# Kernel optimization log

Measured on AMD Instinct MI355X. Metric: run time of the kernel, lower is better.

The kernel has to match this reference:

```python
import jax, jax.numpy as jnp
import numpy as np

H = 4  # num_heads


def _ln(x, g, b, eps=1e-5):
    m = x.mean(-1, keepdims=True)
    v = ((x - m) ** 2).mean(-1, keepdims=True)
    return (x - m) / jnp.sqrt(v + eps) * g + b


def setup_inputs() -> dict:
    key = jax.random.key(0)
    ks = jax.random.split(key, 16)
    B, N, M, dQ, dK, dV = 4, 2048, 2048, 128, 128, 128
    s = 0.02
    return {
        "Q": jax.random.normal(ks[0], (B, N, dQ), jnp.float32),
        "K": jax.random.normal(ks[1], (B, M, dK), jnp.float32),
        "adj_mask": jax.random.randint(ks[2], (B, N, M), 0, 2, jnp.int32),
        "Wq": jax.random.normal(ks[3], (dQ, dV), jnp.float32) * s,
        "bq": jnp.zeros((dV,), jnp.float32),
        "Wk": jax.random.normal(ks[4], (dK, dV), jnp.float32) * s,
        "bk": jnp.zeros((dV,), jnp.float32),
        "Wv": jax.random.normal(ks[5], (dK, dV), jnp.float32) * s,
        "bv": jnp.zeros((dV,), jnp.float32),
        "Wr1": jax.random.normal(ks[6], (dV, dV), jnp.float32) * s,
        "br1": jnp.zeros((dV,), jnp.float32),
        "Wr2": jax.random.normal(ks[7], (dV, dV), jnp.float32) * s,
        "br2": jnp.zeros((dV,), jnp.float32),
        "g0": jnp.ones((dV,), jnp.float32),
        "be0": jnp.zeros((dV,), jnp.float32),
        "g1": jnp.ones((dV,), jnp.float32),
        "be1": jnp.zeros((dV,), jnp.float32),
    }


def reference(Q, K, adj_mask, Wq, bq, Wk, bk, Wv, bv, Wr1, br1, Wr2, br2, g0, be0, g1, be1):
    B, N, _ = Q.shape
    M = K.shape[1]
    dV = Wq.shape[1]
    dh = dV // H
    Qp = Q @ Wq + bq   # [B,N,dV]
    Kp = K @ Wk + bk   # [B,M,dV]
    Vp = K @ Wv + bv   # [B,M,dV]
    # torch: split dim_V into H chunks, cat along dim 0 -> head-major [H*B, L, dh]
    def to_heads(x, L):
        return x.reshape(B, L, H, dh).transpose(2, 0, 1, 3).reshape(H * B, L, dh)
    Qh, Kh, Vh = to_heads(Qp, N), to_heads(Kp, M), to_heads(Vp, M)
    attn = jnp.einsum('bnd,bmd->bnm', Qh, Kh) / jnp.sqrt(jnp.float32(dh))  # [H*B,N,M]
    # torch repeat_interleave(mask, H, dim=0) gives batch-major order -- faithful
    mask = jnp.repeat(adj_mask, H, axis=0)
    attn = jnp.where(mask == 0, -jnp.inf, attn)
    A = jax.nn.softmax(attn, axis=2)
    O = Qh + jnp.einsum('bnm,bmd->bnd', A, Vh)  # [H*B,N,dh]
    # recombine heads back to [B,N,dV] (intended split(dim=0)/cat(dim=2))
    O = O.reshape(H, B, N, dh).transpose(1, 2, 0, 3).reshape(B, N, dV)
    O = _ln(O, g0, be0)
    O = O + (jax.nn.relu(O @ Wr1 + br1) @ Wr2 + br2)
    return _ln(O, g1, be1)
```

## Files before the change

kernel.cpp:

```cpp
#include <hip/hip_runtime.h>
#include <hip/hip_bf16.h>


typedef short bf16x8 __attribute__((ext_vector_type(8)));
typedef float f32x4 __attribute__((ext_vector_type(4)));

#define BN 4
#define SEQ 2048
#define DIM 128
#define NH 4
#define DH 32
#define ROWS (BN * SEQ)
#define MS 4
#define MWORDS (SEQ / 32)

static __device__ __forceinline__ unsigned short f2bf(float f) {
    __hip_bfloat16 h = __float2bfloat16(f);
    return *reinterpret_cast<unsigned short*>(&h);
}
static __device__ __forceinline__ float bf2f(unsigned short u) {
    union { unsigned int i; float f; } cv;
    cv.i = ((unsigned int)u) << 16;
    return cv.f;
}
static __device__ __forceinline__ unsigned int pack2bf(float a, float b) {
    return (unsigned int)f2bf(a) | ((unsigned int)f2bf(b) << 16);
}

__global__ __launch_bounds__(256) void fused_prep(
    const float* __restrict__ Q, const float* __restrict__ K,
    const float* __restrict__ bq, const float* __restrict__ bk,
    const float* __restrict__ bv,
    const float* __restrict__ Wq, const float* __restrict__ Wk,
    const float* __restrict__ Wv, const float* __restrict__ W1,
    const float* __restrict__ W2, const int* __restrict__ adj,
    float* __restrict__ Qp, unsigned short* __restrict__ Qb,
    unsigned short* __restrict__ Kb, unsigned short* __restrict__ Vt,
    unsigned int* __restrict__ bits, unsigned short* __restrict__ WT)
{
    __shared__ __align__(16) unsigned char smem[52288];
    const int bx = blockIdx.x;
    const int t = threadIdx.x;

    if (bx >= 1792) {
        const float* W = (bx == 1792) ? W1 : W2;
        unsigned short* out = WT + (bx - 1792) * DIM * DIM;
        for (int i = t; i < DIM * DIM; i += 256) {
            int n = i >> 7, k = i & 127;
            out[i] = f2bf(W[k * DIM + n]);
        }
        return;
    }

    if (bx >= 768) {
        unsigned int (*sB)[65] = (unsigned int(*)[65])smem;
        const int q0 = (bx - 768) * 8;
#pragma unroll
        for (int i = 0; i < 2; ++i) {
            int widl = i * 256 + t;
            int ql = widl >> 6, wd = widl & 63;
            const int4* src = (const int4*)(adj + (long)(q0 + ql) * SEQ + wd * 32);
            unsigned int w = 0;
#pragma unroll
            for (int j = 0; j < 8; ++j) {
                int4 v = src[j];
                w |= (((unsigned)v.x & 1u) << (4 * j))
                   | (((unsigned)v.y & 1u) << (4 * j + 1))
                   | (((unsigned)v.z & 1u) << (4 * j + 2))
                   | (((unsigned)v.w & 1u) << (4 * j + 3));
            }
            sB[ql][wd] = w;
        }
        __syncthreads();
        const int h = q0 >> 11, qh0 = q0 & 2047;
#pragma unroll
        for (int i = 0; i < 2; ++i) {
            int idx = i * 256 + t;
            int wd = idx >> 3, ql = idx & 7;
            bits[((long)h * MWORDS + wd) * SEQ + qh0 + ql] = sB[ql][wd];
        }
        return;
    }

    unsigned short (*sW)[136] = (unsigned short(*)[136])smem;
    unsigned short (*sX)[136] = (unsigned short(*)[136])(smem + 34816);
    unsigned short (*sY)[137] = (unsigned short(*)[137])(smem + 43520);

    const int proj = bx >> 8;
    const int rowbase = (bx & 255) * 32;
    const float* X = (proj == 0) ? Q : K;
    const float* W = (proj == 0) ? Wq : (proj == 1) ? Wk : Wv;
    const float* bias = (proj == 0) ? bq : (proj == 1) ? bk : bv;
    const int bidx = rowbase >> 11;
    const int srowbase = rowbase & 2047;

#pragma unroll
    for (int i = 0; i < 16; ++i) {
        int idx = i * 256 + t;
        int k = idx >> 5, n4 = (idx & 31) * 4;
        float4 v = *(const float4*)(W + k * DIM + n4);
        sW[n4 + 0][k] = f2bf(v.x);
        sW[n4 + 1][k] = f2bf(v.y);
        sW[n4 + 2][k] = f2bf(v.z);
        sW[n4 + 3][k] = f2bf(v.w);
    }
#pragma unroll
    for (int i = 0; i < 4; ++i) {
        int idx = i * 256 + t;
        int row = idx >> 5, c4 = (idx & 31) * 4;
        float4 v = *(const float4*)(X + (long)(rowbase + row) * DIM + c4);
        sX[row][c4 + 0] = f2bf(v.x);
        sX[row][c4 + 1] = f2bf(v.y);
        sX[row][c4 + 2] = f2bf(v.z);
        sX[row][c4 + 3] = f2bf(v.w);
    }
    __syncthreads();

    const int w = t >> 6, lane = t & 63;
    const int n16 = lane & 15, quad = lane >> 4;

    f32x4 acc[2][2];
#pragma unroll
    for (int r = 0; r < 2; ++r)
#pragma unroll
        for (int ct = 0; ct < 2; ++ct)
            acc[r][ct] = (f32x4){0.f, 0.f, 0.f, 0.f};

    for (int ks = 0; ks < 4; ++ks) {
        bf16x8 bfrag[2];
#pragma unroll
        for (int ct = 0; ct < 2; ++ct) {
            int ncol = w * 32 + ct * 16 + n16;
            bfrag[ct] = *(const bf16x8*)(&sW[ncol][ks * 32 + quad * 8]);
        }
#pragma unroll
        for (int r = 0; r < 2; ++r) {
            bf16x8 afrag = *(const bf16x8*)(&sX[r * 16 + n16][ks * 32 + quad * 8]);
#pragma unroll
            for (int ct = 0; ct < 2; ++ct)
                acc[r][ct] = __builtin_amdgcn_mfma_f32_16x16x32_bf16(
                    afrag, bfrag[ct], acc[r][ct], 0, 0, 0);
        }
    }

#pragma unroll
    for (int r = 0; r < 2; ++r) {
#pragma unroll
        for (int ct = 0; ct < 2; ++ct) {
            int col = w * 32 + ct * 16 + n16;
            int hh = col >> 5, dd = col & 31;
            float bv_ = bias[col];
#pragma unroll
            for (int i = 0; i < 4; ++i) {
                int lrow = r * 16 + quad * 4 + i;
                int grow = rowbase + lrow;
                int srow = srowbase + lrow;
                float val = acc[r][ct][i] + bv_;
                if (proj == 0) {
                    Qp[(long)grow * DIM + col] = val;
                    Qb[((long)(hh * BN + bidx) * SEQ + srow) * DH + dd]
                        = f2bf(val * 0.17677669529663687f);
                } else if (proj == 1) {
                    Kb[((long)(hh * BN + bidx) * SEQ + srow) * DH + dd] = f2bf(val);
                } else {
                    sY[lrow][col] = f2bf(val);
                }
            }
        }
    }
    if (proj == 2) {
        __syncthreads();
#pragma unroll
        for (int i = 0; i < 16; ++i) {
            int idx = i * 256 + t;
            int c = idx >> 5, m = idx & 31;
            Vt[((long)bidx * DIM + c) * SEQ + srowbase + m] = sY[m][c];
        }
    }
}

__global__ __launch_bounds__(256, 2) void attn_kernel(
    const unsigned short* __restrict__ Qb, const unsigned short* __restrict__ Kb,
    const unsigned short* __restrict__ Vt, const unsigned int* __restrict__ mbits,
    unsigned short* __restrict__ Opart, float* __restrict__ Lpart)
{
    __shared__ __align__(16) unsigned short sP[4][32][68];

    const int id = blockIdx.x;
    const int combo = id & 15;
    const int qidx = id >> 4;
    const int h = combo >> 2;
    const int sp = combo & 3;
    const int qbase = qidx * 32;
    const int t = threadIdx.x;
    const int b = t >> 6;
    const int lane = t & 63, n16 = lane & 15, quad = lane >> 4;

    const unsigned short* Qh = Qb + ((long)(h * BN + b) * SEQ) * DH + quad * 8;
    const unsigned short* Kp = Kb + ((long)(h * BN + b) * SEQ) * DH + quad * 8;
    const unsigned short* Vp = Vt + ((long)b * DIM + h * DH) * SEQ + quad * 8;
    const unsigned int*   Mp = mbits + ((long)h * MWORDS + sp * 16) * SEQ + qbase + n16;

    bf16x8 qfrag[2];
#pragma unroll
    for (int r = 0; r < 2; ++r)
        qfrag[r] = *(const bf16x8*)(Qh + (long)(qbase + r * 16 + n16) * DH);

    f32x4 o[2][2];
    float lsum[2];
#pragma unroll
    for (int r = 0; r < 2; ++r) {
#pragma unroll
        for (int ct = 0; ct < 2; ++ct) o[r][ct] = (f32x4){0.f, 0.f, 0.f, 0.f};
        lsum[r] = 0.f;
    }

    bf16x8 kf[2][2];
    unsigned int mw[2][2];
    const int mb0 = sp * 512;

#pragma unroll
    for (int c = 0; c < 2; ++c)
        kf[0][c] = *(const bf16x8*)(Kp + (long)(mb0 + c * 16 + n16) * DH);
#pragma unroll
    for (int r = 0; r < 2; ++r) mw[0][r] = Mp[r * 16];

    const f32x4 zero4 = {0.f, 0.f, 0.f, 0.f};

#pragma unroll
    for (int mt = 0; mt < 16; ++mt) {
        const int cur = mt & 1, nxt = cur ^ 1;
        const int mbc = mb0 + mt * 32;
        bf16x8 vf0 = *(const bf16x8*)(Vp + (long)(0 * 16 + n16) * SEQ + mbc);
        bf16x8 vf1 = *(const bf16x8*)(Vp + (long)(1 * 16 + n16) * SEQ + mbc);
        if (mt < 15) {
            const int mb = mbc + 32;
#pragma unroll
            for (int c = 0; c < 2; ++c)
                kf[nxt][c] = *(const bf16x8*)(Kp + (long)(mb + c * 16 + n16) * DH);
#pragma unroll
            for (int r = 0; r < 2; ++r) mw[nxt][r] = Mp[(long)(mt + 1) * SEQ + r * 16];
        }
#pragma unroll
        for (int r = 0; r < 2; ++r) {
            f32x4 st[2];
#pragma unroll
            for (int c = 0; c < 2; ++c)
                st[c] = __builtin_amdgcn_mfma_f32_16x16x32_bf16(
                    kf[cur][c], qfrag[r], zero4, 0, 0, 0);
            const unsigned int wm = mw[cur][r];
            float p[2][4];
#pragma unroll
            for (int c = 0; c < 2; ++c)
#pragma unroll
                for (int i = 0; i < 4; ++i) {
                    float e = __expf(st[c][i]);
                    p[c][i] = ((wm >> (c * 16 + quad * 4 + i)) & 1u) ? e : 0.f;
                    lsum[r] += p[c][i];
                }
#pragma unroll
            for (int c = 0; c < 2; ++c) {
                uint2 wv;
                wv.x = pack2bf(p[c][0], p[c][1]);
                wv.y = pack2bf(p[c][2], p[c][3]);
                *(uint2*)&sP[b][r * 16 + n16][c * 16 + quad * 4] = wv;
            }
        }
#pragma unroll
        for (int r = 0; r < 2; ++r) {
            bf16x8 pa = *(const bf16x8*)(&sP[b][r * 16 + n16][quad * 8]);
            o[r][0] = __builtin_amdgcn_mfma_f32_16x16x32_bf16(pa, vf0, o[r][0], 0, 0, 0);
            o[r][1] = __builtin_amdgcn_mfma_f32_16x16x32_bf16(pa, vf1, o[r][1], 0, 0, 0);
        }
    }

#pragma unroll
    for (int r = 0; r < 2; ++r) {
        lsum[r] += __shfl_xor(lsum[r], 16, 64);
        lsum[r] += __shfl_xor(lsum[r], 32, 64);
    }

#pragma unroll
    for (int r = 0; r < 2; ++r)
#pragma unroll
        for (int ct = 0; ct < 2; ++ct)
#pragma unroll
            for (int i = 0; i < 4; ++i)
                sP[b][r * 16 + quad * 4 + i][ct * 16 + n16] = f2bf(o[r][ct][i]);
    {
        const uint4 w0 = *(const uint4*)&sP[b][lane >> 1][(lane & 1) * 16];
        const uint4 w1 = *(const uint4*)&sP[b][lane >> 1][(lane & 1) * 16 + 8];
        unsigned short* Ob = Opart
            + ((((long)sp * NH + h) * BN + b) * SEQ + qbase) * 32;
        *(uint4*)(Ob + (long)lane * 16)     = w0;
        *(uint4*)(Ob + (long)lane * 16 + 8) = w1;
    }

    if (quad == 0) {
#pragma unroll
        for (int r = 0; r < 2; ++r)
            Lpart[(((long)sp * BN + b) * NH + h) * SEQ + qbase + r * 16 + n16] = lsum[r];
    }
}

__global__ __launch_bounds__(256) void epi_kernel(
    const float* __restrict__ Qp, const unsigned short* __restrict__ Opart,
    const float* __restrict__ Lpart, const unsigned short* __restrict__ WT,
    const float* __restrict__ br1, const float* __restrict__ br2,
    const float* __restrict__ g0, const float* __restrict__ be0,
    const float* __restrict__ g1, const float* __restrict__ be1,
    float* __restrict__ out)
{
    __shared__ __align__(16) unsigned short sXb[16][136];
    __shared__ __align__(16) unsigned short sHb[16][136];
    __shared__ __align__(16) float sXf[16][132];

    const int rowbase = blockIdx.x * 16;
    const int t = threadIdx.x;
    const int row = t >> 4, col8 = (t & 15) * 8;
    const int grow = rowbase + row;
    const int bidx = grow >> 11;
    const int srow = grow & 2047;
    const int head = col8 >> 5;
    const int dd = col8 & 31;

    {
        float l = 0.f;
#pragma unroll
        for (int s = 0; s < MS; ++s)
            l += Lpart[(((long)s * BN + bidx) * NH + head) * SEQ + srow];
        float linv = 1.f / l;

        float ovf[8];
#pragma unroll
        for (int j = 0; j < 8; ++j) ovf[j] = 0.f;
#pragma unroll
        for (int s = 0; s < MS; ++s) {
            bf16x8 p = *(const bf16x8*)(Opart
                + ((((long)s * NH + head) * BN + bidx) * SEQ + srow) * 32 + dd);
#pragma unroll
            for (int j = 0; j < 8; ++j) ovf[j] += bf2f((unsigned short)p[j]);
        }

        float vals[8];
        float sum = 0.f, ss = 0.f;
#pragma unroll
        for (int j = 0; j < 8; j += 4) {
            float4 qv = *(const float4*)(Qp + (long)grow * DIM + col8 + j);
            vals[j + 0] = qv.x + ovf[j + 0] * linv;
            vals[j + 1] = qv.y + ovf[j + 1] * linv;
            vals[j + 2] = qv.z + ovf[j + 2] * linv;
            vals[j + 3] = qv.w + ovf[j + 3] * linv;
#pragma unroll
            for (int u = 0; u < 4; ++u) { sum += vals[j + u]; ss += vals[j + u] * vals[j + u]; }
        }
        sum += __shfl_xor(sum, 1, 64); sum += __shfl_xor(sum, 2, 64);
        sum += __shfl_xor(sum, 4, 64); sum += __shfl_xor(sum, 8, 64);
        ss  += __shfl_xor(ss, 1, 64);  ss  += __shfl_xor(ss, 2, 64);
        ss  += __shfl_xor(ss, 4, 64);  ss  += __shfl_xor(ss, 8, 64);
        float mean = sum * (1.f / 128.f);
        float var  = ss * (1.f / 128.f) - mean * mean;
        float rstd = rsqrtf(var + 1e-5f);
#pragma unroll
        for (int j = 0; j < 8; ++j) {
            int col = col8 + j;
            float x = (vals[j] - mean) * rstd * g0[col] + be0[col];
            sXf[row][col] = x;
            sXb[row][col] = f2bf(x);
        }
    }
    __syncthreads();

    const int w = t >> 6, lane = t & 63;
    const int n16 = lane & 15, quad = lane >> 4;
    const unsigned short* W1t = WT;
    const unsigned short* W2t = WT + DIM * DIM;

    f32x4 acc[2];
#pragma unroll
    for (int ct = 0; ct < 2; ++ct) acc[ct] = (f32x4){0.f, 0.f, 0.f, 0.f};
    for (int ks = 0; ks < 4; ++ks) {
        bf16x8 afrag = *(const bf16x8*)(&sXb[n16][ks * 32 + quad * 8]);
#pragma unroll
        for (int ct = 0; ct < 2; ++ct) {
            bf16x8 bfrag = *(const bf16x8*)(W1t + (w * 32 + ct * 16 + n16) * DIM + ks * 32 + quad * 8);
            acc[ct] = __builtin_amdgcn_mfma_f32_16x16x32_bf16(afrag, bfrag, acc[ct], 0, 0, 0);
        }
    }
#pragma unroll
    for (int ct = 0; ct < 2; ++ct) {
        int col = w * 32 + ct * 16 + n16;
        float bb = br1[col];
#pragma unroll
        for (int i = 0; i < 4; ++i) {
            float hv = acc[ct][i] + bb;
            sHb[quad * 4 + i][col] = f2bf(fmaxf(hv, 0.f));
        }
    }
    __syncthreads();

    f32x4 acc2[2];
#pragma unroll
    for (int ct = 0; ct < 2; ++ct) acc2[ct] = (f32x4){0.f, 0.f, 0.f, 0.f};
    for (int ks = 0; ks < 4; ++ks) {
        bf16x8 afrag = *(const bf16x8*)(&sHb[n16][ks * 32 + quad * 8]);
#pragma unroll
        for (int ct = 0; ct < 2; ++ct) {
            bf16x8 bfrag = *(const bf16x8*)(W2t + (w * 32 + ct * 16 + n16) * DIM + ks * 32 + quad * 8);
            acc2[ct] = __builtin_amdgcn_mfma_f32_16x16x32_bf16(afrag, bfrag, acc2[ct], 0, 0, 0);
        }
    }
    float yv[2][4];
#pragma unroll
    for (int ct = 0; ct < 2; ++ct) {
        int col = w * 32 + ct * 16 + n16;
        float bb = br2[col];
#pragma unroll
        for (int i = 0; i < 4; ++i)
            yv[ct][i] = acc2[ct][i] + bb + sXf[quad * 4 + i][col];
    }
    __syncthreads();
#pragma unroll
    for (int ct = 0; ct < 2; ++ct) {
        int col = w * 32 + ct * 16 + n16;
#pragma unroll
        for (int i = 0; i < 4; ++i)
            sXf[quad * 4 + i][col] = yv[ct][i];
    }
    __syncthreads();

    {
        float vals[8];
        float sum = 0.f, ss = 0.f;
#pragma unroll
        for (int j = 0; j < 8; ++j) {
            float v = sXf[row][col8 + j];
            vals[j] = v; sum += v; ss += v * v;
        }
        sum += __shfl_xor(sum, 1, 64); sum += __shfl_xor(sum, 2, 64);
        sum += __shfl_xor(sum, 4, 64); sum += __shfl_xor(sum, 8, 64);
        ss  += __shfl_xor(ss, 1, 64);  ss  += __shfl_xor(ss, 2, 64);
        ss  += __shfl_xor(ss, 4, 64);  ss  += __shfl_xor(ss, 8, 64);
        float mean = sum * (1.f / 128.f);
        float var  = ss * (1.f / 128.f) - mean * mean;
        float rstd = rsqrtf(var + 1e-5f);
        float* op = out + (long)grow * DIM + col8;
#pragma unroll
        for (int j = 0; j < 8; j += 4) {
            float4 ov;
            int col = col8 + j;
            ov.x = (vals[j + 0] - mean) * rstd * g1[col + 0] + be1[col + 0];
            ov.y = (vals[j + 1] - mean) * rstd * g1[col + 1] + be1[col + 1];
            ov.z = (vals[j + 2] - mean) * rstd * g1[col + 2] + be1[col + 2];
            ov.w = (vals[j + 3] - mean) * rstd * g1[col + 3] + be1[col + 3];
            *(float4*)(op + j) = ov;
        }
    }
}

extern "C" void kernel_launch(void* const* d_in, const int* in_sizes, int n_in,
                              void* d_out, int out_size, void* d_ws, size_t ws_size,
                              hipStream_t stream) {
    const float* Q   = (const float*)d_in[0];
    const float* K   = (const float*)d_in[1];
    const int*   adj = (const int*)d_in[2];
    const float* Wq  = (const float*)d_in[3];
    const float* bq  = (const float*)d_in[4];
    const float* Wk  = (const float*)d_in[5];
    const float* bk  = (const float*)d_in[6];
    const float* Wv  = (const float*)d_in[7];
    const float* bv  = (const float*)d_in[8];
    const float* Wr1 = (const float*)d_in[9];
    const float* br1 = (const float*)d_in[10];
    const float* Wr2 = (const float*)d_in[11];
    const float* br2 = (const float*)d_in[12];
    const float* g0  = (const float*)d_in[13];
    const float* be0 = (const float*)d_in[14];
    const float* g1  = (const float*)d_in[15];
    const float* be1 = (const float*)d_in[16];
    float* out = (float*)d_out;

    float* Qp             = (float*)d_ws;
    unsigned short* Opart = (unsigned short*)(Qp + (long)ROWS * DIM);
    float* Lpart          = (float*)(Opart + (long)MS * ROWS * DIM);
    unsigned short* Qb    = (unsigned short*)(Lpart + (long)MS * BN * NH * SEQ);
    unsigned short* Kb    = Qb + (long)ROWS * DIM;
    unsigned short* Vt    = Kb + (long)ROWS * DIM;
    unsigned short* WT    = Vt + (long)ROWS * DIM;
    unsigned int*   bits  = (unsigned int*)(WT + 2 * DIM * DIM);

    fused_prep<<<1794, 256, 0, stream>>>(Q, K, bq, bk, bv, Wq, Wk, Wv, Wr1, Wr2,
                                         adj, Qp, Qb, Kb, Vt, bits, WT);
    attn_kernel<<<1024, 256, 0, stream>>>(Qb, Kb, Vt, bits, Opart, Lpart);
    epi_kernel<<<512, 256, 0, stream>>>(Qp, Opart, Lpart, WT, br1, br2,
                                        g0, be0, g1, be1, out);
}
```

Baseline: 178.8 us.

## Read int32 adjacency mask directly in attention, dropping bit-packing prep stage

Removes the prep blocks that packed the int32 adjacency mask into bit words. The attention kernel now loads int4 mask chunks straight from the original array, double-buffered alongside the K fragments. This cuts the bitmask write and re-read and shrinks the prep launch. In exchange the attention loop moves far more mask bytes per tile, and the four warps of a block load the same mask rows redundantly, so more cache and register pressure lands inside the compute loop.

After: 197.2 us. +10.3%, slower.

```diff
diff --git a/kernel.cpp b/kernel.cpp
--- a/kernel.cpp
+++ b/kernel.cpp
@@ -12,7 +12,6 @@
 #define DH 32
 #define ROWS (BN * SEQ)
 #define MS 4
-#define MWORDS (SEQ / 32)
 
 static __device__ __forceinline__ unsigned short f2bf(float f) {
     __hip_bfloat16 h = __float2bfloat16(f);
@@ -27,57 +26,27 @@
     return (unsigned int)f2bf(a) | ((unsigned int)f2bf(b) << 16);
 }
 
-__global__ __launch_bounds__(256) void fused_prep(
+__global__ __launch_bounds__(256) void proj_prep(
     const float* __restrict__ Q, const float* __restrict__ K,
     const float* __restrict__ bq, const float* __restrict__ bk,
     const float* __restrict__ bv,
     const float* __restrict__ Wq, const float* __restrict__ Wk,
     const float* __restrict__ Wv, const float* __restrict__ W1,
-    const float* __restrict__ W2, const int* __restrict__ adj,
+    const float* __restrict__ W2,
     float* __restrict__ Qp, unsigned short* __restrict__ Qb,
     unsigned short* __restrict__ Kb, unsigned short* __restrict__ Vt,
-    unsigned int* __restrict__ bits, unsigned short* __restrict__ WT)
+    unsigned short* __restrict__ WT)
 {
     __shared__ __align__(16) unsigned char smem[52288];
     const int bx = blockIdx.x;
     const int t = threadIdx.x;
 
-    if (bx >= 1792) {
-        const float* W = (bx == 1792) ? W1 : W2;
-        unsigned short* out = WT + (bx - 1792) * DIM * DIM;
+    if (bx >= 768) {
+        const float* W = (bx == 768) ? W1 : W2;
+        unsigned short* out = WT + (bx - 768) * DIM * DIM;
         for (int i = t; i < DIM * DIM; i += 256) {
             int n = i >> 7, k = i & 127;
             out[i] = f2bf(W[k * DIM + n]);
-        }
-        return;
-    }
-
-    if (bx >= 768) {
-        unsigned int (*sB)[65] = (unsigned int(*)[65])smem;
-        const int q0 = (bx - 768) * 8;
-#pragma unroll
-        for (int i = 0; i < 2; ++i) {
-            int widl = i * 256 + t;
-            int ql = widl >> 6, wd = widl & 63;
-            const int4* src = (const int4*)(adj + (long)(q0 + ql) * SEQ + wd * 32);
-            unsigned int w = 0;
-#pragma unroll
-            for (int j = 0; j < 8; ++j) {
-                int4 v = src[j];
-                w |= (((unsigned)v.x & 1u) << (4 * j))
-                   | (((unsigned)v.y & 1u) << (4 * j + 1))
-                   | (((unsigned)v.z & 1u) << (4 * j + 2))
-                   | (((unsigned)v.w & 1u) << (4 * j + 3));
-            }
-            sB[ql][wd] = w;
-        }
-        __syncthreads();
-        const int h = q0 >> 11, qh0 = q0 & 2047;
-#pragma unroll
-        for (int i = 0; i < 2; ++i) {
-            int idx = i * 256 + t;
-            int wd = idx >> 3, ql = idx & 7;
-            bits[((long)h * MWORDS + wd) * SEQ + qh0 + ql] = sB[ql][wd];
         }
         return;
     }
@@ -181,7 +150,7 @@
 
 __global__ __launch_bounds__(256, 2) void attn_kernel(
     const unsigned short* __restrict__ Qb, const unsigned short* __restrict__ Kb,
-    const unsigned short* __restrict__ Vt, const unsigned int* __restrict__ mbits,
+    const unsigned short* __restrict__ Vt, const int* __restrict__ adj,
     unsigned short* __restrict__ Opart, float* __restrict__ Lpart)
 {
     __shared__ __align__(16) unsigned short sP[4][32][68];
@@ -199,7 +168,10 @@
     const unsigned short* Qh = Qb + ((long)(h * BN + b) * SEQ) * DH + quad * 8;
     const unsigned short* Kp = Kb + ((long)(h * BN + b) * SEQ) * DH + quad * 8;
     const unsigned short* Vp = Vt + ((long)b * DIM + h * DH) * SEQ + quad * 8;
-    const unsigned int*   Mp = mbits + ((long)h * MWORDS + sp * 16) * SEQ + qbase + n16;
+    const int* Mr[2];
+#pragma unroll
+    for (int r = 0; r < 2; ++r)
+        Mr[r] = adj + ((long)h * SEQ + qbase + r * 16 + n16) * SEQ + quad * 4;
 
     bf16x8 qfrag[2];
 #pragma unroll
@@ -216,14 +188,17 @@
     }
 
     bf16x8 kf[2][2];
-    unsigned int mw[2][2];
+    int4 mk[2][2][2];
     const int mb0 = sp * 512;
 
 #pragma unroll
     for (int c = 0; c < 2; ++c)
         kf[0][c] = *(const bf16x8*)(Kp + (long)(mb0 + c * 16 + n16) * DH);
 #pragma unroll
-    for (int r = 0; r < 2; ++r) mw[0][r] = Mp[r * 16];
+    for (int r = 0; r < 2; ++r)
+#pragma unroll
+        for (int c = 0; c < 2; ++c)
+            mk[0][r][c] = *(const int4*)(Mr[r] + mb0 + c * 16);
 
     const f32x4 zero4 = {0.f, 0.f, 0.f, 0.f};
 
@@ -239,7 +214,10 @@
             for (int c = 0; c < 2; ++c)
                 kf[nxt][c] = *(const bf16x8*)(Kp + (long)(mb + c * 16 + n16) * DH);
 #pragma unroll
-            for (int r = 0; r < 2; ++r) mw[nxt][r] = Mp[(long)(mt + 1) * SEQ + r * 16];
+            for (int r = 0; r < 2; ++r)
+#pragma unroll
+                for (int c = 0; c < 2; ++c)
+                    mk[nxt][r][c] = *(const int4*)(Mr[r] + mb + c * 16);
         }
 #pragma unroll
         for (int r = 0; r < 2; ++r) {
@@ -248,16 +226,17 @@
             for (int c = 0; c < 2; ++c)
                 st[c] = __builtin_amdgcn_mfma_f32_16x16x32_bf16(
                     kf[cur][c], qfrag[r], zero4, 0, 0, 0);
-            const unsigned int wm = mw[cur][r];
             float p[2][4];
 #pragma unroll
-            for (int c = 0; c < 2; ++c)
+            for (int c = 0; c < 2; ++c) {
+                const int* mp = (const int*)&mk[cur][r][c];
 #pragma unroll
                 for (int i = 0; i < 4; ++i) {
                     float e = __expf(st[c][i]);
-                    p[c][i] = ((wm >> (c * 16 + quad * 4 + i)) & 1u) ? e : 0.f;
+                    p[c][i] = mp[i] ? e : 0.f;
                     lsum[r] += p[c][i];
                 }
+            }
 #pragma unroll
             for (int c = 0; c < 2; ++c) {
                 uint2 wv;
@@ -487,11 +466,10 @@
     unsigned short* Kb    = Qb + (long)ROWS * DIM;
     unsigned short* Vt    = Kb + (long)ROWS * DIM;
     unsigned short* WT    = Vt + (long)ROWS * DIM;
-    unsigned int*   bits  = (unsigned int*)(WT + 2 * DIM * DIM);
-
-    fused_prep<<<1794, 256, 0, stream>>>(Q, K, bq, bk, bv, Wq, Wk, Wv, Wr1, Wr2,
-                                         adj, Qp, Qb, Kb, Vt, bits, WT);
-    attn_kernel<<<1024, 256, 0, stream>>>(Qb, Kb, Vt, bits, Opart, Lpart);
+
+    proj_prep<<<770, 256, 0, stream>>>(Q, K, bq, bk, bv, Wq, Wk, Wv, Wr1, Wr2,
+                                       Qp, Qb, Kb, Vt, WT);
+    attn_kernel<<<1024, 256, 0, stream>>>(Qb, Kb, Vt, adj, Opart, Lpart);
     epi_kernel<<<512, 256, 0, stream>>>(Qp, Opart, Lpart, WT, br1, br2,
                                         g0, be0, g1, be1, out);
 }
```
